# Kernel optimization log

Hardware: AMD Instinct MI355X
Metric: run time of the kernel (lower is better)

## Reference

```python
import jax, jax.numpy as jnp
import numpy as np
from jax import lax


def _demap(yr, amp, logp, sigma):
    # Gaussian soft demapper over K amplitude levels, per real dimension.
    d = yr[..., None] - amp  # [..., K]
    return jax.nn.softmax(-d * d / (2.0 * sigma * sigma) + logp, axis=-1)


def _cfull(a, b, Loff, N):
    # full convolution then the idx = [2*Loff, N) window used by the tap loop
    return jnp.convolve(a, b, mode='full')[2 * Loff:N]


def _elbo(y_blk, q, amp, h_est, p_amps, sps):
    # y_blk: [2, N, 2] (re/im), q: [2, B, 2K], h_est: [2, 2, 2, L]
    N = y_blk.shape[1]
    L = h_est.shape[-1]
    Loff = (L - 1) // 2
    K = amp.shape[0]
    E0 = q[:, :, :K] @ amp      # [2, B] E[x] in-phase
    E1 = q[:, :, K:] @ amp      # [2, B] E[x] quadrature
    a2 = amp * amp
    V = q[:, :, :K] @ a2 + q[:, :, K:] @ a2 - E0 ** 2 - E1 ** 2  # [2, B]
    EQ = jnp.zeros((2, 2, N), q.dtype).at[:, 0, ::sps].set(E0).at[:, 1, ::sps].set(E1)
    Var = jnp.zeros((2, N), q.dtype).at[:, ::sps].set(V)
    # D term: the explicit tap loop over j with gathers EQ[..., idx-j] is a
    # 2x2 complex convolution of EQ with h_est, restricted to idx=[2*Loff, N)
    Dr = jnp.stack([
        sum(_cfull(EQ[i, 0], h_est[p, i, 0], Loff, N) - _cfull(EQ[i, 1], h_est[p, i, 1], Loff, N)
            for i in range(2)) for p in range(2)])
    Di = jnp.stack([
        sum(_cfull(EQ[i, 0], h_est[p, i, 1], Loff, N) + _cfull(EQ[i, 1], h_est[p, i, 0], Loff, N)
            for i in range(2)) for p in range(2)])
    # E term: sliding window sums of Var via cumsum
    h_absq = jnp.sum(h_est ** 2, axis=2)  # [2, 2, L]
    cs = jnp.concatenate([jnp.zeros((2, 1), Var.dtype), jnp.cumsum(Var, axis=1)], axis=1)
    js = jnp.arange(L)
    Wsum = cs[:, N - js] - cs[:, 2 * Loff - js]  # [2, L], sum_n Var[i, idx-j]
    E = jnp.einsum('pil,il->p', h_absq, Wsum)
    p_rep = jnp.concatenate([p_amps, p_amps])
    qs = q[:, Loff:-Loff, :]
    A = jnp.sum(qs * jnp.log(qs / p_rep + 1e-14), axis=(1, 2))
    yr = y_blk[:, Loff:N - Loff, 0]
    yi = y_blk[:, Loff:N - Loff, 1]
    C = jnp.sum(yr ** 2 + yi ** 2, axis=1)
    C = C - 2.0 * jnp.sum(yr * Dr + yi * Di, axis=1) + jnp.sum(Dr ** 2 + Di ** 2, axis=1) + E
    loss = jnp.sum(A) + (N - L + 1) * jnp.sum(jnp.log(C + 1e-8))
    var = C / (N - L + 1)
    return loss, var


def _forward(y, taps, h_est, amp_levels, p_symbols, noise_sigma, sps, block_size):
    T = taps.shape[2]
    pad = (T - 1) // 2
    num_samps = y.shape[1]
    step = sps * block_size
    nb = (num_samps - 2 * pad - 1) // step  # == len(range(pad, num_samps-pad-step, step))
    starts = pad + step * jnp.arange(nb)
    W = step + 2 * pad
    idx = starts[:, None] + jnp.arange(W)[None, :] - pad  # [nb, W]
    win = y[:, idx]  # [2, nb, W, 2]
    xr = jnp.transpose(win[..., 0], (1, 0, 2))  # [nb, 2, W]
    xi = jnp.transpose(win[..., 1], (1, 0, 2))
    wr = taps[..., 0]
    wi = taps[..., 1]
    conv = lambda x, w: lax.conv_general_dilated(x, w, (1,), 'VALID', dimension_numbers=('NCH', 'OIH', 'NCH'))
    # 2x2 complex butterfly FIR (cross-correlation like torch conv1d), 'valid'
    yhr = conv(xr, wr) - conv(xi, wi)  # [nb, 2, step]
    yhi = conv(xr, wi) + conv(xi, wr)
    ysr = yhr[:, :, ::sps]  # [nb, 2, B]
    ysi = yhi[:, :, ::sps]
    sigma = noise_sigma[0]
    logp = jnp.log(p_symbols)
    q = jnp.concatenate([_demap(ysr, amp_levels, logp, sigma),
                         _demap(ysi, amp_levels, logp, sigma)], axis=-1)  # [nb, 2, B, 2K]
    yidx = starts[:, None] + jnp.arange(step)[None, :]
    y_blocks = jnp.transpose(y[:, yidx], (1, 0, 2, 3))  # [nb, 2, step, 2]
    losses, vars_ = jax.vmap(lambda yb, qb: _elbo(yb, qb, amp_levels, h_est, p_symbols, sps))(y_blocks, q)
    out_y = jnp.stack([ysr, ysi], axis=-1)  # [nb, 2, B, 2]
    out_y = jnp.transpose(out_y, (1, 0, 2, 3)).reshape(2, nb * block_size, 2)
    out_q = jnp.transpose(q, (1, 0, 2, 3)).reshape(2, nb * block_size, -1)
    return out_y, out_q, vars_[-1], losses


def setup_inputs() -> dict:
    key = jax.random.key(0)
    k0, k1, k2 = jax.random.split(key, 3)
    pad = 32  # (65-1)//2
    num_samps = 2 * pad + 4096 * 513  # 512 blocks of sps*block_size=4096
    y = jax.random.normal(k0, (2, num_samps, 2), jnp.float32)
    taps = jax.random.normal(k1, (2, 2, 65, 2), jnp.float32) * 0.05
    taps = taps.at[0, 0, 32, 0].add(1.0).at[1, 1, 32, 0].add(1.0)
    h_est = jax.random.normal(k2, (2, 2, 2, 25), jnp.float32) * 0.05
    h_est = h_est.at[0, 0, 0, 13].add(1.0).at[1, 1, 0, 13].add(1.0)  # torch init: ones at L//2+1
    a = jnp.arange(16, dtype=jnp.float32)
    amp = 2.0 * a - 15.0
    amp = amp / jnp.sqrt(jnp.mean(amp ** 2))  # unit-power ASK levels (256-QAM per dim)
    p_symbols = jnp.ones((16,), jnp.float32) / 16.0
    noise_sigma = jnp.array([0.5], jnp.float32)
    return {"y": y, "taps": taps, "h_est": h_est, "amp_levels": amp,
            "p_symbols": p_symbols, "noise_sigma": noise_sigma, "sps": 2, "block_size": 2048}


def reference(y, taps, h_est, amp_levels, p_symbols, noise_sigma, sps, block_size):
    return _forward(y, taps, h_est, amp_levels, p_symbols, noise_sigma, sps, block_size)
```

## Files before the change

kernel.cpp:

```cpp
#include <hip/hip_runtime.h>

#define NB      512
#define NSAMP   2101312L
#define SOUT    2048
#define LOFF    12
#define NEDGE   12
#define NJ      4072
#define CHUNK   512
#define NCHUNK  4
#define STAGE   544

#define OUTY_OFF   0
#define OUTQ_OFF   4194304L
#define OUTVAR_OFF (4194304L + 67108864L)

__global__ __launch_bounds__(512, 4)
void vae_elbo_kernel(const float* __restrict__ y,
                     const float* __restrict__ taps,
                     const float* __restrict__ h_est,
                     const float* __restrict__ amp,
                     const float* __restrict__ p_sym,
                     const float* __restrict__ nsig,
                     float* __restrict__ out)
{
    const int k   = blockIdx.x;
    const int tid = threadIdx.x;
    const long Bk = (long)k * 4096;

    float* const out_y    = out + OUTY_OFF;
    float* const out_q    = out + OUTQ_OFF;
    float* const out_var  = out + OUTVAR_OFF;
    float* const out_loss = out + OUTVAR_OFF + 2;

    __shared__ float xer[2][STAGE], xei[2][STAGE];
    __shared__ float xodr[2][STAGE], xodi[2][STAGE];
    __shared__ float E0L[2][SOUT], E1L[2][SOUT];
    __shared__ float Vlo[2][NEDGE], Vhi[2][NEDGE];
    __shared__ float red[8][12];

    const float sg = nsig[0];
    const float inv2s2 = 1.0f / (2.0f * sg * sg);

    float amps[16], ivp[16];
    #pragma unroll
    for (int c = 0; c < 16; ++c) {
        amps[c] = amp[c];
        ivp[c]  = 1.0f / p_sym[c];
    }

    float kl_acc = 0.0f;
    float vt0 = 0.0f, vt1 = 0.0f;

    for (int cn = 0; cn < NCHUNK; ++cn) {
        const int s0 = cn * CHUNK;
        __syncthreads();
        {
            const float4* y4 = (const float4*)y;
            #pragma unroll
            for (int it = 0; it < 3; ++it) {
                int idx = tid + it * 512;
                if (idx < 2 * STAGE) {
                    int i = (idx >= STAGE) ? 1 : 0;
                    int u = idx - i * STAGE;
                    float4 v = y4[(((long)i * NSAMP + Bk) >> 1) + s0 + u];
                    xer[i][u]  = v.x; xei[i][u]  = v.y;
                    xodr[i][u] = v.z; xodi[i][u] = v.w;
                }
            }
        }
        __syncthreads();

        const int s = s0 + tid;

        float ar0 = 0.f, ai0 = 0.f, ar1 = 0.f, ai1 = 0.f;
        #pragma unroll
        for (int i = 0; i < 2; ++i) {
            const float* tA = taps + i * 130;
            const float* tB = taps + 260 + i * 130;
            #pragma unroll
            for (int m = 0; m <= 32; ++m) {
                float xr = xer[i][tid + m], xi = xei[i][tid + m];
                float wr = tA[4*m], wi = tA[4*m + 1];
                ar0 = fmaf(xr, wr, ar0); ar0 = fmaf(-xi, wi, ar0);
                ai0 = fmaf(xr, wi, ai0); ai0 = fmaf( xi, wr, ai0);
                wr = tB[4*m]; wi = tB[4*m + 1];
                ar1 = fmaf(xr, wr, ar1); ar1 = fmaf(-xi, wi, ar1);
                ai1 = fmaf(xr, wi, ai1); ai1 = fmaf( xi, wr, ai1);
            }
            #pragma unroll
            for (int m = 0; m < 32; ++m) {
                float xr = xodr[i][tid + m], xi = xodi[i][tid + m];
                float wr = tA[4*m + 2], wi = tA[4*m + 3];
                ar0 = fmaf(xr, wr, ar0); ar0 = fmaf(-xi, wi, ar0);
                ai0 = fmaf(xr, wi, ai0); ai0 = fmaf( xi, wr, ai0);
                wr = tB[4*m + 2]; wi = tB[4*m + 3];
                ar1 = fmaf(xr, wr, ar1); ar1 = fmaf(-xi, wi, ar1);
                ai1 = fmaf(xr, wi, ai1); ai1 = fmaf( xi, wr, ai1);
            }
        }

        #pragma unroll
        for (int o = 0; o < 2; ++o) {
            const float yhr = o ? ar1 : ar0;
            const float yhi = o ? ai1 : ai0;

            float qv[32];
            float E0 = 0.f, E1 = 0.f, Vs = 0.f;
            {
                float z[16], zm = -3.0e38f;
                #pragma unroll
                for (int c = 0; c < 16; ++c) {
                    float d = yhr - amps[c];
                    z[c] = -d * d * inv2s2;
                    zm = fmaxf(zm, z[c]);
                }
                float se = 0.f;
                #pragma unroll
                for (int c = 0; c < 16; ++c) { z[c] = __expf(z[c] - zm); se += z[c]; }
                float inv = 1.0f / se;
                #pragma unroll
                for (int c = 0; c < 16; ++c) {
                    float q = z[c] * inv;
                    qv[c] = q;
                    E0 = fmaf(q, amps[c], E0);
                    Vs = fmaf(q, amps[c] * amps[c], Vs);
                }
            }
            {
                float z[16], zm = -3.0e38f;
                #pragma unroll
                for (int c = 0; c < 16; ++c) {
                    float d = yhi - amps[c];
                    z[c] = -d * d * inv2s2;
                    zm = fmaxf(zm, z[c]);
                }
                float se = 0.f;
                #pragma unroll
                for (int c = 0; c < 16; ++c) { z[c] = __expf(z[c] - zm); se += z[c]; }
                float inv = 1.0f / se;
                #pragma unroll
                for (int c = 0; c < 16; ++c) {
                    float q = z[c] * inv;
                    qv[16 + c] = q;
                    E1 = fmaf(q, amps[c], E1);
                    Vs = fmaf(q, amps[c] * amps[c], Vs);
                }
            }
            Vs = Vs - E0 * E0 - E1 * E1;

            E0L[o][s] = E0;
            E1L[o][s] = E1;
            if (o == 0) vt0 += Vs; else vt1 += Vs;
            if (s < NEDGE)          Vlo[o][s] = Vs;
            if (s >= SOUT - NEDGE)  Vhi[o][s - (SOUT - NEDGE)] = Vs;

            if (s >= LOFF && s < SOUT - LOFF) {
                float klp = 0.f;
                #pragma unroll
                for (int c = 0; c < 32; ++c)
                    klp += qv[c] * __logf(fmaf(qv[c], ivp[c & 15], 1e-14f));
                kl_acc += klp;
            }

            const long gy = ((long)(o * NB + k)) * SOUT + s;
            ((float2*)out_y)[gy] = make_float2(yhr, yhi);
            float4* oq = (float4*)(out_q + gy * 32);
            #pragma unroll
            for (int w = 0; w < 8; ++w)
                oq[w] = make_float4(qv[4*w], qv[4*w+1], qv[4*w+2], qv[4*w+3]);
        }
    }
    __syncthreads();

    float sy2[2] = {0.f, 0.f}, syd[2] = {0.f, 0.f}, sd2[2] = {0.f, 0.f};
    const float2* y2 = (const float2*)y;
    #pragma unroll
    for (int par = 0; par < 2; ++par) {
        const int mcnt = 13 - par;
        for (int r = 0; r < 4; ++r) {
            const int t2 = tid + r * 512;
            if (t2 < SOUT - LOFF) {
                const int j  = 2 * t2 + par;
                const int sb = t2 + LOFF;
                float dr0 = 0.f, di0 = 0.f, dr1 = 0.f, di1 = 0.f;
                #pragma unroll
                for (int i = 0; i < 2; ++i) {
                    #pragma unroll
                    for (int m = 0; m < mcnt; ++m) {
                        const int l = 2 * m + par;
                        const float e0 = E0L[i][sb - m];
                        const float e1 = E1L[i][sb - m];
                        float hr = h_est[((0 * 2 + i) * 2 + 0) * 25 + l];
                        float hi = h_est[((0 * 2 + i) * 2 + 1) * 25 + l];
                        dr0 += e0 * hr - e1 * hi;
                        di0 += e0 * hi + e1 * hr;
                        hr = h_est[((1 * 2 + i) * 2 + 0) * 25 + l];
                        hi = h_est[((1 * 2 + i) * 2 + 1) * 25 + l];
                        dr1 += e0 * hr - e1 * hi;
                        di1 += e0 * hi + e1 * hr;
                    }
                }
                float2 yv = y2[Bk + 44 + j];
                sy2[0] += yv.x * yv.x + yv.y * yv.y;
                syd[0] += yv.x * dr0 + yv.y * di0;
                sd2[0] += dr0 * dr0 + di0 * di0;
                yv = y2[NSAMP + Bk + 44 + j];
                sy2[1] += yv.x * yv.x + yv.y * yv.y;
                syd[1] += yv.x * dr1 + yv.y * di1;
                sd2[1] += dr1 * dr1 + di1 * di1;
            }
        }
    }

    float vals[9] = {kl_acc, vt0, vt1, sy2[0], sy2[1], syd[0], syd[1], sd2[0], sd2[1]};
    #pragma unroll
    for (int d = 32; d >= 1; d >>= 1) {
        #pragma unroll
        for (int v = 0; v < 9; ++v)
            vals[v] += __shfl_down(vals[v], (unsigned)d, 64);
    }
    const int wv = tid >> 6;
    if ((tid & 63) == 0) {
        #pragma unroll
        for (int v = 0; v < 9; ++v) red[wv][v] = vals[v];
    }
    __syncthreads();

    if (tid == 0) {
        float tot[9];
        #pragma unroll
        for (int v = 0; v < 9; ++v) {
            float t = 0.f;
            #pragma unroll
            for (int w = 0; w < 8; ++w) t += red[w][v];
            tot[v] = t;
        }
        float Et0 = 0.f, Et1 = 0.f;
        #pragma unroll
        for (int i = 0; i < 2; ++i) {
            const float Vt = (i == 0) ? tot[1] : tot[2];
            float plo[13], phi[13];
            plo[0] = 0.f; phi[0] = 0.f;
            #pragma unroll
            for (int t = 0; t < 12; ++t) {
                plo[t + 1] = plo[t] + Vlo[i][t];
                phi[t + 1] = phi[t] + Vhi[i][11 - t];
            }
            #pragma unroll
            for (int l = 0; l < 25; ++l) {
                int lo, hi;
                if ((l & 1) == 0) { lo = 12 - l / 2;     hi = l / 2; }
                else             { lo = (25 - l) / 2;    hi = (l - 1) / 2; }
                const float ws = Vt - plo[lo] - phi[hi];
                const float h00 = h_est[((0 * 2 + i) * 2 + 0) * 25 + l];
                const float h01 = h_est[((0 * 2 + i) * 2 + 1) * 25 + l];
                const float h10 = h_est[((1 * 2 + i) * 2 + 0) * 25 + l];
                const float h11 = h_est[((1 * 2 + i) * 2 + 1) * 25 + l];
                Et0 += (h00 * h00 + h01 * h01) * ws;
                Et1 += (h10 * h10 + h11 * h11) * ws;
            }
        }
        const float C0 = tot[3] - 2.0f * tot[5] + tot[7] + Et0;
        const float C1 = tot[4] - 2.0f * tot[6] + tot[8] + Et1;
        const float loss = tot[0] + 4072.0f * (logf(C0 + 1e-8f) + logf(C1 + 1e-8f));
        out_loss[k] = loss;
        if (k == NB - 1) {
            out_var[0] = C0 / 4072.0f;
            out_var[1] = C1 / 4072.0f;
        }
    }
}

extern "C" void kernel_launch(void* const* d_in, const int* in_sizes, int n_in,
                              void* d_out, int out_size, void* d_ws, size_t ws_size,
                              hipStream_t stream) {
    const float* y     = (const float*)d_in[0];
    const float* taps  = (const float*)d_in[1];
    const float* h_est = (const float*)d_in[2];
    const float* amp   = (const float*)d_in[3];
    const float* p_sym = (const float*)d_in[4];
    const float* nsig  = (const float*)d_in[5];
    (void)in_sizes; (void)n_in; (void)out_size; (void)d_ws; (void)ws_size;

    vae_elbo_kernel<<<NB, 512, 0, stream>>>(y, taps, h_est, amp, p_sym, nsig,
                                            (float*)d_out);
}
```

Measured before the change: 1.185 ms.

## Process two output samples per thread and fuse demap, KL and D-term passes

Each thread now computes two output positions per chunk, with chunks of 1024 instead of 512, so every tap weight load feeds twice as many FMAs. Staging buffers move to float2 LDS layout. The demapper is restructured into a lambda that streams q straight to global memory and fuses the KL term, which avoids holding a 32-entry q array. The D-term loop handles even and odd phases in one pass, sharing each E load and reading y as float4. This should cut scalar and shared-memory load overhead per FLOP, but raises register pressure under the launch bound of 512 threads and 4 blocks.

```diff
diff --git a/kernel.cpp b/kernel.cpp
--- a/kernel.cpp
+++ b/kernel.cpp
@@ -4,11 +4,10 @@
 #define NSAMP   2101312L
 #define SOUT    2048
 #define LOFF    12
-#define NEDGE   12
 #define NJ      4072
-#define CHUNK   512
-#define NCHUNK  4
-#define STAGE   544
+#define CHUNK   1024
+#define NCHUNK  2
+#define XSTG    1056
 
 #define OUTY_OFF   0
 #define OUTQ_OFF   4194304L
@@ -32,183 +31,177 @@
     float* const out_var  = out + OUTVAR_OFF;
     float* const out_loss = out + OUTVAR_OFF + 2;
 
-    __shared__ float xer[2][STAGE], xei[2][STAGE];
-    __shared__ float xodr[2][STAGE], xodi[2][STAGE];
-    __shared__ float E0L[2][SOUT], E1L[2][SOUT];
-    __shared__ float Vlo[2][NEDGE], Vhi[2][NEDGE];
-    __shared__ float red[8][12];
+    __shared__ float2 xe[2][XSTG];
+    __shared__ float2 xo[2][XSTG];
+    __shared__ float2 EL[2][SOUT];
+    __shared__ float  Vlo[2][LOFF], Vhi[2][LOFF];
+    __shared__ float  red[8][12];
 
     const float sg = nsig[0];
     const float inv2s2 = 1.0f / (2.0f * sg * sg);
 
-    float amps[16], ivp[16];
-    #pragma unroll
-    for (int c = 0; c < 16; ++c) {
-        amps[c] = amp[c];
-        ivp[c]  = 1.0f / p_sym[c];
-    }
-
     float kl_acc = 0.0f;
     float vt0 = 0.0f, vt1 = 0.0f;
 
+    auto demap16 = [&](float yh, float* qdst, float& Eo, float& Vs, float& klp,
+                       bool doKL) {
+        float z[16];
+        float zm = -3.0e38f;
+        #pragma unroll
+        for (int c = 0; c < 16; ++c) {
+            float d = yh - amp[c];
+            z[c] = -d * d * inv2s2;
+            zm = fmaxf(zm, z[c]);
+        }
+        float se = 0.f;
+        #pragma unroll
+        for (int c = 0; c < 16; ++c) { z[c] = __expf(z[c] - zm); se += z[c]; }
+        const float inv = 1.0f / se;
+        #pragma unroll
+        for (int c = 0; c < 16; ++c) {
+            float q = z[c] * inv;
+            z[c] = q;
+            float t = q * amp[c];
+            Eo += t;
+            Vs = fmaf(t, amp[c], Vs);
+            if (doKL) {
+                const float ip = 1.0f / p_sym[c];
+                klp += q * __logf(fmaf(q, ip, 1e-14f));
+            }
+        }
+        #pragma unroll
+        for (int w = 0; w < 4; ++w)
+            ((float4*)qdst)[w] = make_float4(z[4*w], z[4*w+1], z[4*w+2], z[4*w+3]);
+    };
+
+    #pragma unroll 1
     for (int cn = 0; cn < NCHUNK; ++cn) {
         const int s0 = cn * CHUNK;
         __syncthreads();
         {
             const float4* y4 = (const float4*)y;
             #pragma unroll
-            for (int it = 0; it < 3; ++it) {
+            for (int it = 0; it < 5; ++it) {
                 int idx = tid + it * 512;
-                if (idx < 2 * STAGE) {
-                    int i = (idx >= STAGE) ? 1 : 0;
-                    int u = idx - i * STAGE;
+                if (idx < 2 * XSTG) {
+                    int i = (idx >= XSTG) ? 1 : 0;
+                    int u = idx - i * XSTG;
                     float4 v = y4[(((long)i * NSAMP + Bk) >> 1) + s0 + u];
-                    xer[i][u]  = v.x; xei[i][u]  = v.y;
-                    xodr[i][u] = v.z; xodi[i][u] = v.w;
+                    xe[i][u] = make_float2(v.x, v.y);
+                    xo[i][u] = make_float2(v.z, v.w);
                 }
             }
         }
         __syncthreads();
 
-        const int s = s0 + tid;
-
-        float ar0 = 0.f, ai0 = 0.f, ar1 = 0.f, ai1 = 0.f;
+        float arA0=0.f, aiA0=0.f, arA1=0.f, aiA1=0.f;
+        float arB0=0.f, aiB0=0.f, arB1=0.f, aiB1=0.f;
         #pragma unroll
         for (int i = 0; i < 2; ++i) {
             const float* tA = taps + i * 130;
             const float* tB = taps + 260 + i * 130;
             #pragma unroll
             for (int m = 0; m <= 32; ++m) {
-                float xr = xer[i][tid + m], xi = xei[i][tid + m];
+                float2 ea = xe[i][tid + m];
+                float2 eb = xe[i][tid + 512 + m];
                 float wr = tA[4*m], wi = tA[4*m + 1];
-                ar0 = fmaf(xr, wr, ar0); ar0 = fmaf(-xi, wi, ar0);
-                ai0 = fmaf(xr, wi, ai0); ai0 = fmaf( xi, wr, ai0);
+                arA0 = fmaf(ea.x, wr, arA0); arA0 = fmaf(-ea.y, wi, arA0);
+                aiA0 = fmaf(ea.x, wi, aiA0); aiA0 = fmaf( ea.y, wr, aiA0);
+                arB0 = fmaf(eb.x, wr, arB0); arB0 = fmaf(-eb.y, wi, arB0);
+                aiB0 = fmaf(eb.x, wi, aiB0); aiB0 = fmaf( eb.y, wr, aiB0);
                 wr = tB[4*m]; wi = tB[4*m + 1];
-                ar1 = fmaf(xr, wr, ar1); ar1 = fmaf(-xi, wi, ar1);
-                ai1 = fmaf(xr, wi, ai1); ai1 = fmaf( xi, wr, ai1);
+                arA1 = fmaf(ea.x, wr, arA1); arA1 = fmaf(-ea.y, wi, arA1);
+                aiA1 = fmaf(ea.x, wi, aiA1); aiA1 = fmaf( ea.y, wr, aiA1);
+                arB1 = fmaf(eb.x, wr, arB1); arB1 = fmaf(-eb.y, wi, arB1);
+                aiB1 = fmaf(eb.x, wi, aiB1); aiB1 = fmaf( eb.y, wr, aiB1);
             }
             #pragma unroll
             for (int m = 0; m < 32; ++m) {
-                float xr = xodr[i][tid + m], xi = xodi[i][tid + m];
+                float2 oa = xo[i][tid + m];
+                float2 ob = xo[i][tid + 512 + m];
                 float wr = tA[4*m + 2], wi = tA[4*m + 3];
-                ar0 = fmaf(xr, wr, ar0); ar0 = fmaf(-xi, wi, ar0);
-                ai0 = fmaf(xr, wi, ai0); ai0 = fmaf( xi, wr, ai0);
+                arA0 = fmaf(oa.x, wr, arA0); arA0 = fmaf(-oa.y, wi, arA0);
+                aiA0 = fmaf(oa.x, wi, aiA0); aiA0 = fmaf( oa.y, wr, aiA0);
+                arB0 = fmaf(ob.x, wr, arB0); arB0 = fmaf(-ob.y, wi, arB0);
+                aiB0 = fmaf(ob.x, wi, aiB0); aiB0 = fmaf( ob.y, wr, aiB0);
                 wr = tB[4*m + 2]; wi = tB[4*m + 3];
-                ar1 = fmaf(xr, wr, ar1); ar1 = fmaf(-xi, wi, ar1);
-                ai1 = fmaf(xr, wi, ai1); ai1 = fmaf( xi, wr, ai1);
-            }
-        }
-
-        #pragma unroll
-        for (int o = 0; o < 2; ++o) {
-            const float yhr = o ? ar1 : ar0;
-            const float yhi = o ? ai1 : ai0;
-
-            float qv[32];
-            float E0 = 0.f, E1 = 0.f, Vs = 0.f;
-            {
-                float z[16], zm = -3.0e38f;
+                arA1 = fmaf(oa.x, wr, arA1); arA1 = fmaf(-oa.y, wi, arA1);
+                aiA1 = fmaf(oa.x, wi, aiA1); aiA1 = fmaf( oa.y, wr, aiA1);
+                arB1 = fmaf(ob.x, wr, arB1); arB1 = fmaf(-ob.y, wi, arB1);
+                aiB1 = fmaf(ob.x, wi, aiB1); aiB1 = fmaf( ob.y, wr, aiB1);
+            }
+        }
+
+        #pragma unroll
+        for (int j = 0; j < 2; ++j) {
+            const int sgb = s0 + tid + j * 512;
+            const bool doKL = (sgb >= LOFF) && (sgb < SOUT - LOFF);
+            #pragma unroll
+            for (int o = 0; o < 2; ++o) {
+                const float yhr = o ? (j ? arB1 : arA1) : (j ? arB0 : arA0);
+                const float yhi = o ? (j ? aiB1 : aiA1) : (j ? aiB0 : aiA0);
+                float E0 = 0.f, E1 = 0.f, Vs = 0.f, klp = 0.f;
+                const long gy = ((long)(o * NB + k)) * SOUT + sgb;
+                demap16(yhr, out_q + gy * 32,      E0, Vs, klp, doKL);
+                demap16(yhi, out_q + gy * 32 + 16, E1, Vs, klp, doKL);
+                Vs -= E0 * E0 + E1 * E1;
+
+                EL[o][sgb] = make_float2(E0, E1);
+                if (o == 0) vt0 += Vs; else vt1 += Vs;
+                if (sgb < LOFF)          Vlo[o][sgb] = Vs;
+                if (sgb >= SOUT - LOFF)  Vhi[o][sgb - (SOUT - LOFF)] = Vs;
+                kl_acc += klp;
+
+                ((float2*)out_y)[gy] = make_float2(yhr, yhi);
+            }
+        }
+    }
+    __syncthreads();
+
+    float sy2[2] = {0.f, 0.f}, syd[2] = {0.f, 0.f}, sd2[2] = {0.f, 0.f};
+    #pragma unroll 1
+    for (int r = 0; r < 4; ++r) {
+        const int t2 = tid + r * 512;
+        if (t2 < SOUT - LOFF) {
+            float dr0e=0.f, di0e=0.f, dr1e=0.f, di1e=0.f;
+            float dr0o=0.f, di0o=0.f, dr1o=0.f, di1o=0.f;
+            #pragma unroll
+            for (int i = 0; i < 2; ++i) {
                 #pragma unroll
-                for (int c = 0; c < 16; ++c) {
-                    float d = yhr - amps[c];
-                    z[c] = -d * d * inv2s2;
-                    zm = fmaxf(zm, z[c]);
-                }
-                float se = 0.f;
-                #pragma unroll
-                for (int c = 0; c < 16; ++c) { z[c] = __expf(z[c] - zm); se += z[c]; }
-                float inv = 1.0f / se;
-                #pragma unroll
-                for (int c = 0; c < 16; ++c) {
-                    float q = z[c] * inv;
-                    qv[c] = q;
-                    E0 = fmaf(q, amps[c], E0);
-                    Vs = fmaf(q, amps[c] * amps[c], Vs);
-                }
-            }
-            {
-                float z[16], zm = -3.0e38f;
-                #pragma unroll
-                for (int c = 0; c < 16; ++c) {
-                    float d = yhi - amps[c];
-                    z[c] = -d * d * inv2s2;
-                    zm = fmaxf(zm, z[c]);
-                }
-                float se = 0.f;
-                #pragma unroll
-                for (int c = 0; c < 16; ++c) { z[c] = __expf(z[c] - zm); se += z[c]; }
-                float inv = 1.0f / se;
-                #pragma unroll
-                for (int c = 0; c < 16; ++c) {
-                    float q = z[c] * inv;
-                    qv[16 + c] = q;
-                    E1 = fmaf(q, amps[c], E1);
-                    Vs = fmaf(q, amps[c] * amps[c], Vs);
-                }
-            }
-            Vs = Vs - E0 * E0 - E1 * E1;
-
-            E0L[o][s] = E0;
-            E1L[o][s] = E1;
-            if (o == 0) vt0 += Vs; else vt1 += Vs;
-            if (s < NEDGE)          Vlo[o][s] = Vs;
-            if (s >= SOUT - NEDGE)  Vhi[o][s - (SOUT - NEDGE)] = Vs;
-
-            if (s >= LOFF && s < SOUT - LOFF) {
-                float klp = 0.f;
-                #pragma unroll
-                for (int c = 0; c < 32; ++c)
-                    klp += qv[c] * __logf(fmaf(qv[c], ivp[c & 15], 1e-14f));
-                kl_acc += klp;
-            }
-
-            const long gy = ((long)(o * NB + k)) * SOUT + s;
-            ((float2*)out_y)[gy] = make_float2(yhr, yhi);
-            float4* oq = (float4*)(out_q + gy * 32);
-            #pragma unroll
-            for (int w = 0; w < 8; ++w)
-                oq[w] = make_float4(qv[4*w], qv[4*w+1], qv[4*w+2], qv[4*w+3]);
-        }
-    }
-    __syncthreads();
-
-    float sy2[2] = {0.f, 0.f}, syd[2] = {0.f, 0.f}, sd2[2] = {0.f, 0.f};
-    const float2* y2 = (const float2*)y;
-    #pragma unroll
-    for (int par = 0; par < 2; ++par) {
-        const int mcnt = 13 - par;
-        for (int r = 0; r < 4; ++r) {
-            const int t2 = tid + r * 512;
-            if (t2 < SOUT - LOFF) {
-                const int j  = 2 * t2 + par;
-                const int sb = t2 + LOFF;
-                float dr0 = 0.f, di0 = 0.f, dr1 = 0.f, di1 = 0.f;
-                #pragma unroll
-                for (int i = 0; i < 2; ++i) {
-                    #pragma unroll
-                    for (int m = 0; m < mcnt; ++m) {
-                        const int l = 2 * m + par;
-                        const float e0 = E0L[i][sb - m];
-                        const float e1 = E1L[i][sb - m];
-                        float hr = h_est[((0 * 2 + i) * 2 + 0) * 25 + l];
-                        float hi = h_est[((0 * 2 + i) * 2 + 1) * 25 + l];
-                        dr0 += e0 * hr - e1 * hi;
-                        di0 += e0 * hi + e1 * hr;
-                        hr = h_est[((1 * 2 + i) * 2 + 0) * 25 + l];
-                        hi = h_est[((1 * 2 + i) * 2 + 1) * 25 + l];
-                        dr1 += e0 * hr - e1 * hi;
-                        di1 += e0 * hi + e1 * hr;
+                for (int m = 0; m <= 12; ++m) {
+                    const float2 el = EL[i][t2 + 12 - m];
+                    {
+                        const int l = 2 * m;
+                        float h0r = h_est[((0*2 + i)*2 + 0)*25 + l];
+                        float h0i = h_est[((0*2 + i)*2 + 1)*25 + l];
+                        float h1r = h_est[((1*2 + i)*2 + 0)*25 + l];
+                        float h1i = h_est[((1*2 + i)*2 + 1)*25 + l];
+                        dr0e = fmaf(el.x, h0r, dr0e); dr0e = fmaf(-el.y, h0i, dr0e);
+                        di0e = fmaf(el.x, h0i, di0e); di0e = fmaf( el.y, h0r, di0e);
+                        dr1e = fmaf(el.x, h1r, dr1e); dr1e = fmaf(-el.y, h1i, dr1e);
+                        di1e = fmaf(el.x, h1i, di1e); di1e = fmaf( el.y, h1r, di1e);
+                    }
+                    if (m < 12) {
+                        const int l = 2 * m + 1;
+                        float h0r = h_est[((0*2 + i)*2 + 0)*25 + l];
+                        float h0i = h_est[((0*2 + i)*2 + 1)*25 + l];
+                        float h1r = h_est[((1*2 + i)*2 + 0)*25 + l];
+                        float h1i = h_est[((1*2 + i)*2 + 1)*25 + l];
+                        dr0o = fmaf(el.x, h0r, dr0o); dr0o = fmaf(-el.y, h0i, dr0o);
+                        di0o = fmaf(el.x, h0i, di0o); di0o = fmaf( el.y, h0r, di0o);
+                        dr1o = fmaf(el.x, h1r, dr1o); dr1o = fmaf(-el.y, h1i, dr1o);
+                        di1o = fmaf(el.x, h1i, di1o); di1o = fmaf( el.y, h1r, di1o);
                     }
                 }
-                float2 yv = y2[Bk + 44 + j];
-                sy2[0] += yv.x * yv.x + yv.y * yv.y;
-                syd[0] += yv.x * dr0 + yv.y * di0;
-                sd2[0] += dr0 * dr0 + di0 * di0;
-                yv = y2[NSAMP + Bk + 44 + j];
-                sy2[1] += yv.x * yv.x + yv.y * yv.y;
-                syd[1] += yv.x * dr1 + yv.y * di1;
-                sd2[1] += dr1 * dr1 + di1 * di1;
-            }
+            }
+            float4 yv = *(const float4*)&y[(Bk + 44 + 2*t2) * 2];
+            sy2[0] += yv.x*yv.x + yv.y*yv.y + yv.z*yv.z + yv.w*yv.w;
+            syd[0] += yv.x*dr0e + yv.y*di0e + yv.z*dr0o + yv.w*di0o;
+            sd2[0] += dr0e*dr0e + di0e*di0e + dr0o*dr0o + di0o*di0o;
+            yv = *(const float4*)&y[(NSAMP + Bk + 44 + 2*t2) * 2];
+            sy2[1] += yv.x*yv.x + yv.y*yv.y + yv.z*yv.z + yv.w*yv.w;
+            syd[1] += yv.x*dr1e + yv.y*di1e + yv.z*dr1o + yv.w*di1o;
+            sd2[1] += dr1e*dr1e + di1e*di1e + dr1o*dr1o + di1o*di1o;
         }
     }
 
@@ -252,10 +245,10 @@
                 if ((l & 1) == 0) { lo = 12 - l / 2;     hi = l / 2; }
                 else             { lo = (25 - l) / 2;    hi = (l - 1) / 2; }
                 const float ws = Vt - plo[lo] - phi[hi];
-                const float h00 = h_est[((0 * 2 + i) * 2 + 0) * 25 + l];
-                const float h01 = h_est[((0 * 2 + i) * 2 + 1) * 25 + l];
-                const float h10 = h_est[((1 * 2 + i) * 2 + 0) * 25 + l];
-                const float h11 = h_est[((1 * 2 + i) * 2 + 1) * 25 + l];
+                const float h00 = h_est[((0*2 + i)*2 + 0)*25 + l];
+                const float h01 = h_est[((0*2 + i)*2 + 1)*25 + l];
+                const float h10 = h_est[((1*2 + i)*2 + 0)*25 + l];
+                const float h11 = h_est[((1*2 + i)*2 + 1)*25 + l];
                 Et0 += (h00 * h00 + h01 * h01) * ws;
                 Et1 += (h10 * h10 + h11 * h11) * ws;
             }
```

New measurement: 2.076 ms. 1.75x slower.
